# Kernel tuning notes

Measured on AMD Instinct MI355X. Metric: run time of the kernel, lower is better.

Reference implementation:

```python
import jax, jax.numpy as jnp
import numpy as np

B, L, T, V = 64, 512, 1000, 256
E, H, M, S = 256, 512, 80, 128  # text_embed, hidden, n_mels, speaker_dim


def lstm_scan(x, Wih, Whh, b):
    # x: [T, B, D]; torch gate order i, f, g, o; bias = b_ih + b_hh fused
    Bn = x.shape[1]
    Hn = Whh.shape[1]
    h0 = jnp.zeros((Bn, Hn), x.dtype)

    def step(carry, xt):
        h, c = carry
        g = xt @ Wih.T + h @ Whh.T + b
        i, f, gg, o = jnp.split(g, 4, axis=-1)
        c = jax.nn.sigmoid(f) * c + jax.nn.sigmoid(i) * jnp.tanh(gg)
        h = jax.nn.sigmoid(o) * jnp.tanh(c)
        return (h, c), h

    _, ys = jax.lax.scan(step, (h0, h0), x)
    return ys  # [T, B, H]


def setup_inputs() -> dict:
    key = jax.random.key(0)
    ks = jax.random.split(key, 32)
    r = lambda i, shp: (jax.random.normal(ks[i], shp, jnp.float32) * 0.1)
    Hd = H // 2  # 256, per-direction biLSTM hidden
    inp = {
        "text_input": jax.random.randint(ks[0], (B, L), 0, V),
        "speaker_embedding": jax.random.normal(ks[1], (B, S), jnp.float32),
        "target_mel": jax.random.normal(ks[2], (B, T, M), jnp.float32),
        "embed": r(3, (V, E)),
        # bidirectional text LSTM (hidden//2 per direction)
        "enc_Wih_f": r(4, (4 * Hd, E)), "enc_Whh_f": r(5, (4 * Hd, Hd)), "enc_b_f": r(6, (4 * Hd,)),
        "enc_Wih_b": r(7, (4 * Hd, E)), "enc_Whh_b": r(8, (4 * Hd, Hd)), "enc_b_b": r(9, (4 * Hd,)),
        # speaker projection MLP
        "sp_W1": r(10, (H, S)), "sp_b1": r(11, (H,)),
        "sp_W2": r(12, (H, H)), "sp_b2": r(13, (H,)),
        # 2-layer decoder LSTM, input = H + M = 592
        "dec_Wih0": r(14, (4 * H, H + M)), "dec_Whh0": r(15, (4 * H, H)), "dec_b0": r(16, (4 * H,)),
        "dec_Wih1": r(17, (4 * H, H)), "dec_Whh1": r(18, (4 * H, H)), "dec_b1": r(19, (4 * H,)),
        # mel projection MLP
        "mel_W1": r(20, (H, H)), "mel_b1": r(21, (H,)),
        "mel_W2": r(22, (M, H)), "mel_b2": r(23, (M,)),
        # stop token projection
        "stop_W": r(24, (1, H)), "stop_b": r(25, (1,)),
    }
    return inp


def reference(text_input, speaker_embedding, target_mel, embed,
              enc_Wih_f, enc_Whh_f, enc_b_f, enc_Wih_b, enc_Whh_b, enc_b_b,
              sp_W1, sp_b1, sp_W2, sp_b2,
              dec_Wih0, dec_Whh0, dec_b0, dec_Wih1, dec_Whh1, dec_b1,
              mel_W1, mel_b1, mel_W2, mel_b2, stop_W, stop_b):
    # --- text encoder: embedding + biLSTM ---
    x = jnp.swapaxes(embed[text_input], 0, 1)  # [L, B, E]
    fwd = lstm_scan(x, enc_Wih_f, enc_Whh_f, enc_b_f)          # [L, B, H/2]
    bwd = lstm_scan(x[::-1], enc_Wih_b, enc_Whh_b, enc_b_b)[::-1]
    text_encoded = jnp.swapaxes(jnp.concatenate([fwd, bwd], -1), 0, 1)  # [B, L, H]

    # --- speaker projection, broadcast over text length ---
    sp = jax.nn.relu(speaker_embedding @ sp_W1.T + sp_b1) @ sp_W2.T + sp_b2  # [B, H]
    encoder_output = text_encoded + sp[:, None, :]  # [B, L, H]

    # --- teacher-forced decoder: query_t = encoder_output[:, t % L] ---
    idx = jnp.arange(T) % L
    query = encoder_output[:, idx]  # [B, T, H]
    dec_mel_in = jnp.concatenate(
        [jnp.zeros((B, 1, M), target_mel.dtype), target_mel[:, :-1]], axis=1)  # [B, T, M]
    rnn_in = jnp.swapaxes(jnp.concatenate([dec_mel_in, query], -1), 0, 1)  # [T, B, H+M]

    h1 = lstm_scan(rnn_in, dec_Wih0, dec_Whh0, dec_b0)  # [T, B, H]
    h2 = lstm_scan(h1, dec_Wih1, dec_Whh1, dec_b1)      # [T, B, H]
    out = jnp.swapaxes(h2, 0, 1)  # [B, T, H]

    mel_outputs = jax.nn.relu(out @ mel_W1.T + mel_b1) @ mel_W2.T + mel_b2  # [B, T, M]
    stop_outputs = out @ stop_W.T + stop_b  # [B, T, 1]
    return mel_outputs, stop_outputs
```

## Files before the change

kernel.cpp:

```cpp
#include <hip/hip_runtime.h>
#include <cstdint>
#include <cstddef>


#define DEVI __device__ __forceinline__

typedef short bf16x8 __attribute__((ext_vector_type(8)));
typedef float f32x4 __attribute__((ext_vector_type(4)));
typedef unsigned short u16x4 __attribute__((ext_vector_type(4)));

constexpr int B_ = 64, L_ = 512, T_ = 1000, E_ = 256, H_ = 512, M_ = 80, S_ = 128, Hd_ = 256;

DEVI unsigned short f2bs(float f) {
  unsigned u = __builtin_bit_cast(unsigned, f);
  unsigned r = u + 0x7fffu + ((u >> 16) & 1u);
  return (unsigned short)(r >> 16);
}
DEVI float b2f(unsigned short s) { return __builtin_bit_cast(float, (unsigned)s << 16); }
DEVI void split2(float v, unsigned short& hi, unsigned short& lo) {
  hi = f2bs(v);
  lo = f2bs(v - b2f(hi));
}
DEVI float sigm(float x) { x = fminf(fmaxf(x, -30.f), 30.f); return 1.f / (1.f + __expf(-x)); }
DEVI float tanh_(float x) { x = fminf(fmaxf(x, -15.f), 15.f); float e = __expf(2.f * x); return (e - 1.f) / (e + 1.f); }

DEVI f32x4 mfma16(bf16x8 a, bf16x8 b, f32x4 c) {
  return __builtin_amdgcn_mfma_f32_16x16x32_bf16(a, b, c, 0, 0, 0);
}

DEVI void ldg16(bf16x8& r, const unsigned short* p) {
  asm volatile("global_load_dwordx4 %0, %1, off" : "=v"(r) : "v"(p));
}
DEVI void ldc16(bf16x8& r, const unsigned short* p) {
  asm volatile("global_load_dwordx4 %0, %1, off sc0 sc1" : "=v"(r) : "v"(p));
}
DEVI void st4c(unsigned short* p, unsigned v) {
  asm volatile("global_store_dword %0, %1, off sc0 sc1" :: "v"(p), "v"(v));
}
DEVI void sti4c(int* p, int v) {
  asm volatile("global_store_dword %0, %1, off sc0 sc1" :: "v"(p), "v"(v));
}
DEVI void st8c(unsigned short* p, u16x4 v) {
  asm volatile("global_store_dwordx2 %0, %1, off sc0 sc1" :: "v"(p), "v"(v));
}
#define WAITV(N) do { asm volatile("s_waitcnt vmcnt(" #N ")" ::: "memory"); \
                      __builtin_amdgcn_sched_barrier(0); } while (0)
#define VM_DRAIN() WAITV(0)

DEVI void hotwait(const int* p, int target) {
  int v;
  for (;;) {
    asm volatile("global_load_dword %0, %1, off sc0 sc1" : "=v"(v) : "v"(p));
    float x = 0.5f;
#pragma unroll
    for (int i = 0; i < 192; ++i)
      asm volatile("v_fmac_f32 %0, %1, %1" : "+v"(x) : "v"(x));
    asm volatile("" :: "v"(x));
    asm volatile("s_waitcnt vmcnt(0)" ::: "memory");
    __builtin_amdgcn_sched_barrier(0);
    if (v >= target) break;
  }
}

struct Bar { int sub[16][16]; int master[16]; int rel[128][16]; };

template <int NWG, int NSUB>
DEVI void grid_barX(Bar* bb, int step) {
  __shared__ int finS;
  const int tid = threadIdx.x;
  __syncthreads();
  if (tid == 0) {
    finS = 0;
    constexpr int per = NWG / NSUB;
    int old = __hip_atomic_fetch_add(&bb->sub[(int)blockIdx.x % NSUB][0], 1,
                                     __ATOMIC_RELAXED, __HIP_MEMORY_SCOPE_AGENT);
    if (old == per * (step + 1) - 1) {
      int om = __hip_atomic_fetch_add(&bb->master[0], 1,
                                      __ATOMIC_RELAXED, __HIP_MEMORY_SCOPE_AGENT);
      if (om == NSUB * (step + 1) - 1) finS = 1;
    }
  }
  __syncthreads();
  if (finS && tid < NWG) sti4c(&bb->rel[tid][0], step + 1);
  hotwait(&bb->rel[(int)blockIdx.x][0], step + 1);
}

template <int N, class FI, class FM>
DEVI void pipe3(FI issue, FM domf) {
  bf16x8 S0[8], S1[8], S2[8];
  issue(0, S0);
  if constexpr (N > 1) issue(1, S1);
  if constexpr (N > 2) issue(2, S2);
#pragma unroll
  for (int j = 0; j < N; ++j) {
    if (j + 2 < N) { WAITV(16); } else if (j + 1 < N) { WAITV(8); } else { WAITV(0); }
    if (j % 3 == 0)      { domf(j, S0); if (j + 3 < N) issue(j + 3, S0); }
    else if (j % 3 == 1) { domf(j, S1); if (j + 3 < N) issue(j + 3, S1); }
    else                 { domf(j, S2); if (j + 3 < N) issue(j + 3, S2); }
  }
}

__global__ void k_prep(const float* __restrict__ embed, const float* __restrict__ tmel,
                       const float* __restrict__ mw1, const float* __restrict__ mw2,
                       unsigned short* emb_h, unsigned short* emb_l,
                       unsigned short* mel_h, unsigned short* mel_l,
                       unsigned short* w1_bf, unsigned short* w2_bf) {
  const long long stride = (long long)gridDim.x * blockDim.x;
  const long long i0 = (long long)blockIdx.x * blockDim.x + threadIdx.x;
  for (long long i = i0; i < 256 * 256; i += stride) {
    unsigned short h, l; split2(embed[i], h, l);
    emb_h[i] = h; emb_l[i] = l;
  }
  for (long long i = i0; i < (long long)T_ * B_ * 96; i += stride) {
    int c = (int)(i % 96);
    long long tb = i / 96;
    int b = (int)(tb % B_);
    int t = (int)(tb / B_);
    float v = 0.f;
    if (t > 0 && c < 80) v = tmel[((long long)b * T_ + (t - 1)) * M_ + c];
    unsigned short h, l; split2(v, h, l);
    mel_h[i] = h; mel_l[i] = l;
  }
  for (long long i = i0; i < 512 * 512; i += stride) w1_bf[i] = f2bs(mw1[i]);
  for (long long i = i0; i < 80 * 512; i += stride) w2_bf[i] = f2bs(mw2[i]);
}

__global__ void __launch_bounds__(512) k_sp(const float* __restrict__ spk,
                                            const float* __restrict__ w1, const float* __restrict__ b1,
                                            const float* __restrict__ w2, const float* __restrict__ b2,
                                            float* sp) {
  __shared__ float t1[512];
  const int b = blockIdx.x, j = threadIdx.x;
  float a = b1[j];
  const float* sr = spk + b * S_;
  for (int k = 0; k < S_; ++k) a += sr[k] * w1[j * S_ + k];
  t1[j] = fmaxf(a, 0.f);
  __syncthreads();
  float a2 = b2[j];
  for (int k = 0; k < H_; ++k) a2 += t1[k] * w2[j * H_ + k];
  sp[b * H_ + j] = a2;
}

constexpr int ENC_LDS = 2 * 16 * 4 * 64 * 16 + 4 * 64 * 16 * 4 + 256;

__global__ void __launch_bounds__(256, 1) k_enc(
    const int* __restrict__ text,
    const float* __restrict__ WihF, const float* __restrict__ WhhF, const float* __restrict__ bF,
    const float* __restrict__ WihB, const float* __restrict__ WhhB, const float* __restrict__ bB,
    const unsigned short* __restrict__ emb_h, const unsigned short* __restrict__ emb_l,
    const float* __restrict__ sp,
    unsigned short* hencfh, unsigned short* hencfl,
    unsigned short* ench, unsigned short* encl, Bar* bar) {
  extern __shared__ char lds[];
  unsigned short* Wh = (unsigned short*)lds;
  unsigned short* Wl = Wh + 16 * 4 * 64 * 8;
  float* G = (float*)(lds + 2 * 16 * 4 * 64 * 16);
  float* bias = G + 4 * 64 * 16;

  const int wg = blockIdx.x;
  const int dir = wg >> 4;
  const int jhb = (wg & 15) * 16;
  const int tid = threadIdx.x;
  const int wv = tid >> 6, ln = tid & 63, lg = ln >> 4, lr = ln & 15;

  const float* Wih = dir ? WihB : WihF;
  const float* Whh = dir ? WhhB : WhhF;
  const float* bb = dir ? bB : bF;

  for (int s = tid; s < 16 * 4 * 64; s += 256) {
    int kb = s >> 8, g = (s >> 6) & 3, l = s & 63;
    int R = g * Hd_ + jhb + (l & 15);
    int k0 = kb * 32 + (l >> 4) * 8;
    const float* src = (k0 < E_) ? (Wih + (size_t)R * E_ + k0) : (Whh + (size_t)R * Hd_ + (k0 - E_));
    bf16x8 vh, vl;
#pragma unroll
    for (int j = 0; j < 8; ++j) {
      unsigned short a, b; split2(src[j], a, b);
      vh[j] = (short)a; vl[j] = (short)b;
    }
    *(bf16x8*)(Wh + (size_t)s * 8) = vh;
    *(bf16x8*)(Wl + (size_t)s * 8) = vl;
  }
  if (tid < 64) bias[tid] = bb[(tid >> 4) * Hd_ + jhb + (tid & 15)];

  const int eb = tid >> 2, ej0 = (tid & 3) * 4;
  float c4[4] = {0.f, 0.f, 0.f, 0.f};
  float spv[4];
#pragma unroll
  for (int q = 0; q < 4; ++q) spv[q] = sp[eb * H_ + dir * Hd_ + jhb + ej0 + q];

  const int jh = jhb + ej0;
  const size_t fro = ((size_t)((jh >> 5) * 4 + (eb >> 4)) * 64 +
                      (((jh >> 3) & 3) * 16 + (eb & 15))) * 8 + (jh & 7);

  __syncthreads();

  for (int t = 0; t < L_; ++t) {
    const int tpos = dir ? (L_ - 1 - t) : t;
    const unsigned short* hsh = hencfh + ((size_t)((t & 1) * 2 + dir)) * 16384;
    const unsigned short* hsl = hencfl + ((size_t)((t & 1) * 2 + dir)) * 16384;
    unsigned short* hdh = hencfh + ((size_t)(((t + 1) & 1) * 2 + dir)) * 16384;
    unsigned short* hdl = hencfl + ((size_t)(((t + 1) & 1) * 2 + dir)) * 16384;

    for (int i = tid; i < 4096; i += 256) G[i] = bias[((i >> 10) << 4) + (i & 15)];

    int tix[4];
#pragma unroll
    for (int m = 0; m < 4; ++m) tix[m] = text[(16 * m + lr) * L_ + tpos];

    f32x4 acc[4][4];
#pragma unroll
    for (int g = 0; g < 4; ++g)
#pragma unroll
      for (int m = 0; m < 4; ++m) acc[g][m] = (f32x4){0.f, 0.f, 0.f, 0.f};

    auto issue = [&](int j, bf16x8 (&S)[8]) {
      const int kb = wv + 4 * j;
      if (kb < 8) {
        const int k0 = kb * 32 + lg * 8;
#pragma unroll
        for (int m = 0; m < 4; ++m) {
          ldg16(S[m],     emb_h + (size_t)tix[m] * E_ + k0);
          ldg16(S[4 + m], emb_l + (size_t)tix[m] * E_ + k0);
        }
      } else {
        const unsigned short* ph = hsh + ((size_t)((kb - 8) * 4) * 64 + ln) * 8;
        const unsigned short* pl = hsl + ((size_t)((kb - 8) * 4) * 64 + ln) * 8;
#pragma unroll
        for (int m = 0; m < 4; ++m) { ldc16(S[m], ph + m * 512); ldc16(S[4 + m], pl + m * 512); }
      }
    };
    auto domf = [&](int j, bf16x8 (&S)[8]) {
      const int kb = wv + 4 * j;
#pragma unroll
      for (int g = 0; g < 4; ++g) {
        bf16x8 bh = *(bf16x8*)(Wh + ((size_t)(kb * 4 + g) * 64 + ln) * 8);
        bf16x8 bl = *(bf16x8*)(Wl + ((size_t)(kb * 4 + g) * 64 + ln) * 8);
#pragma unroll
        for (int m = 0; m < 4; ++m) {
          acc[g][m] = mfma16(S[m],     bh, acc[g][m]);
          acc[g][m] = mfma16(S[4 + m], bh, acc[g][m]);
          acc[g][m] = mfma16(S[m],     bl, acc[g][m]);
        }
      }
    };
    pipe3<4>(issue, domf);

    __syncthreads();
#pragma unroll
    for (int g = 0; g < 4; ++g)
#pragma unroll
      for (int m = 0; m < 4; ++m)
#pragma unroll
        for (int r = 0; r < 4; ++r)
          atomicAdd(&G[(g * 64 + 16 * m + 4 * lg + r) * 16 + lr], acc[g][m][r]);
    __syncthreads();

    {
      u16x4 hvh, hvl, ovh, ovl;
#pragma unroll
      for (int q = 0; q < 4; ++q) {
        int jj = ej0 + q;
        float gi = G[(0 * 64 + eb) * 16 + jj];
        float gf = G[(1 * 64 + eb) * 16 + jj];
        float gg = G[(2 * 64 + eb) * 16 + jj];
        float go = G[(3 * 64 + eb) * 16 + jj];
        float cn = sigm(gf) * c4[q] + sigm(gi) * tanh_(gg);
        c4[q] = cn;
        float h = sigm(go) * tanh_(cn);
        unsigned short a, b; split2(h, a, b);
        hvh[q] = a; hvl[q] = b;
        float o = h + spv[q];
        split2(o, a, b);
        ovh[q] = a; ovl[q] = b;
      }
      st8c(hdh + fro, hvh);
      st8c(hdl + fro, hvl);
      *(u16x4*)(ench + ((size_t)tpos * B_ + eb) * H_ + dir * Hd_ + jhb + ej0) = ovh;
      *(u16x4*)(encl + ((size_t)tpos * B_ + eb) * H_ + dir * Hd_ + jhb + ej0) = ovl;
    }
    VM_DRAIN();
    grid_barX<32, 8>(bar, t);
  }
}

constexpr int DEC_LDS = 2 * 35 * 2 * 64 * 16 + 4 * 64 * 8 * 4 + 128;

__global__ void __launch_bounds__(256, 1) k_dec(
    const float* __restrict__ Wih0, const float* __restrict__ Whh0, const float* __restrict__ b0,
    const float* __restrict__ Wih1, const float* __restrict__ Whh1, const float* __restrict__ b1,
    const unsigned short* __restrict__ ench, const unsigned short* __restrict__ encl,
    const unsigned short* __restrict__ melh, const unsigned short* __restrict__ mell,
    unsigned short* h0fh, unsigned short* h0fl,
    unsigned short* h1fh, unsigned short* h1fl,
    unsigned short* h2_full, Bar* bar) {
  extern __shared__ char lds[];
  const int wg = blockIdx.x;
  const int layer = wg >> 6;
  const int jcb = (wg & 63) * 8;
  const int tid = threadIdx.x, wv = tid >> 6, ln = tid & 63, lg = ln >> 4, lr = ln & 15;
  const int NKB = layer ? 32 : 35;
  unsigned short* Wh = (unsigned short*)lds;
  unsigned short* Wl = Wh + (size_t)NKB * 2 * 64 * 8;
  float* G = (float*)(lds + (size_t)2 * NKB * 2 * 64 * 16);
  float* bias = G + 4 * 64 * 8;

  if (layer == 0) {
    for (int s = tid; s < 35 * 2 * 64; s += 256) {
      int kb = s >> 7, st = (s >> 6) & 1, l = s & 63;
      int n = l & 15;
      int R = (2 * st + (n >> 3)) * H_ + jcb + (n & 7);
      int k0 = kb * 32 + (l >> 4) * 8;
      bf16x8 vh, vl;
      if (k0 < 96) {
#pragma unroll
        for (int j = 0; j < 8; ++j) {
          int c = k0 + j;
          float v = (c < 80) ? Wih0[(size_t)R * 592 + c] : 0.f;
          unsigned short a, b; split2(v, a, b);
          vh[j] = (short)a; vl[j] = (short)b;
        }
      } else if (k0 < 608) {
        const float* src = Wih0 + (size_t)R * 592 + (k0 - 16);
#pragma unroll
        for (int j = 0; j < 8; ++j) {
          unsigned short a, b; split2(src[j], a, b);
          vh[j] = (short)a; vl[j] = (short)b;
        }
      } else {
        const float* src = Whh0 + (size_t)R * H_ + (k0 - 608);
#pragma unroll
        for (int j = 0; j < 8; ++j) {
          unsigned short a, b; split2(src[j], a, b);
          vh[j] = (short)a; vl[j] = (short)b;
        }
      }
      *(bf16x8*)(Wh + (size_t)s * 8) = vh;
      *(bf16x8*)(Wl + (size_t)s * 8) = vl;
    }
    if (tid < 32) bias[tid] = b0[(tid >> 3) * H_ + jcb + (tid & 7)];
  } else {
    for (int s = tid; s < 32 * 2 * 64; s += 256) {
      int kb = s >> 7, st = (s >> 6) & 1, l = s & 63;
      int n = l & 15;
      int R = (2 * st + (n >> 3)) * H_ + jcb + (n & 7);
      int k0 = kb * 32 + (l >> 4) * 8;
      const float* src = (k0 < 512) ? (Wih1 + (size_t)R * H_ + k0) : (Whh1 + (size_t)R * H_ + (k0 - 512));
      bf16x8 vh, vl;
#pragma unroll
      for (int j = 0; j < 8; ++j) {
        unsigned short a, b; split2(src[j], a, b);
        vh[j] = (short)a; vl[j] = (short)b;
      }
      *(bf16x8*)(Wh + (size_t)s * 8) = vh;
      *(bf16x8*)(Wl + (size_t)s * 8) = vl;
    }
    if (tid < 32) bias[tid] = b1[(tid >> 3) * H_ + jcb + (tid & 7)];
  }

  const int ebd = tid & 63, cc0 = (tid >> 6) * 2;
  float c2[2] = {0.f, 0.f};
  const int j0w = jcb + cc0;
  const size_t frw = ((size_t)((j0w >> 5) * 4 + (ebd >> 4)) * 64 +
                      (((j0w >> 3) & 3) * 16 + (ebd & 15))) * 8 + (j0w & 7);
  __syncthreads();

  for (int tau = 0; tau <= T_; ++tau) {
    const bool active = (layer == 0) ? (tau < T_) : (tau >= 1);
    if (active) {
      const int t = (layer == 0) ? tau : tau - 1;
      for (int i = tid; i < 2048; i += 256) G[i] = bias[((i >> 9) << 3) + (i & 7)];

      f32x4 acc[2][4];
#pragma unroll
      for (int st = 0; st < 2; ++st)
#pragma unroll
        for (int m = 0; m < 4; ++m) acc[st][m] = (f32x4){0.f, 0.f, 0.f, 0.f};

      auto MF = [&](int kb, bf16x8 (&S)[8]) {
#pragma unroll
        for (int st = 0; st < 2; ++st) {
          bf16x8 bh = *(bf16x8*)(Wh + ((size_t)(kb * 2 + st) * 64 + ln) * 8);
          bf16x8 bl = *(bf16x8*)(Wl + ((size_t)(kb * 2 + st) * 64 + ln) * 8);
#pragma unroll
          for (int m = 0; m < 4; ++m) {
            acc[st][m] = mfma16(S[m],     bh, acc[st][m]);
            acc[st][m] = mfma16(S[4 + m], bh, acc[st][m]);
            acc[st][m] = mfma16(S[m],     bl, acc[st][m]);
          }
        }
      };

      if (layer == 0) {
        const int tq = t & (L_ - 1);
        const unsigned short* p0h = h0fh + (size_t)((tau + 1) & 1) * 32768;
        const unsigned short* p0l = h0fl + (size_t)((tau + 1) & 1) * 32768;
        auto issue = [&](int j, bf16x8 (&S)[8]) {
          const int kb = wv + 4 * j;
          const int k0 = kb * 32 + lg * 8;
          if (kb < 3) {
#pragma unroll
            for (int m = 0; m < 4; ++m) {
              ldg16(S[m],     melh + ((size_t)t * B_ + 16 * m + lr) * 96 + k0);
              ldg16(S[4 + m], mell + ((size_t)t * B_ + 16 * m + lr) * 96 + k0);
            }
          } else if (kb < 19) {
            const int k = k0 - 96;
#pragma unroll
            for (int m = 0; m < 4; ++m) {
              ldg16(S[m],     ench + ((size_t)tq * B_ + 16 * m + lr) * H_ + k);
              ldg16(S[4 + m], encl + ((size_t)tq * B_ + 16 * m + lr) * H_ + k);
            }
          } else {
            const unsigned short* ph = p0h + ((size_t)((kb - 19) * 4) * 64 + ln) * 8;
            const unsigned short* pl = p0l + ((size_t)((kb - 19) * 4) * 64 + ln) * 8;
#pragma unroll
            for (int m = 0; m < 4; ++m) { ldc16(S[m], ph + m * 512); ldc16(S[4 + m], pl + m * 512); }
          }
        };
        auto domf = [&](int j, bf16x8 (&S)[8]) { MF(wv + 4 * j, S); };
        if (wv < 3) pipe3<9>(issue, domf);
        else        pipe3<8>(issue, domf);
      } else {
        const unsigned short* q0h = h0fh + (size_t)((tau + 1) & 1) * 32768;
        const unsigned short* q0l = h0fl + (size_t)((tau + 1) & 1) * 32768;
        const unsigned short* q1h = h1fh + (size_t)(tau & 1) * 32768;
        const unsigned short* q1l = h1fl + (size_t)(tau & 1) * 32768;
        auto issue = [&](int j, bf16x8 (&S)[8]) {
          const int kb = wv + 4 * j;
          const unsigned short* ph = (kb < 16) ? (q0h + ((size_t)(kb * 4) * 64 + ln) * 8)
                                               : (q1h + ((size_t)((kb - 16) * 4) * 64 + ln) * 8);
          const unsigned short* pl = (kb < 16) ? (q0l + ((size_t)(kb * 4) * 64 + ln) * 8)
                                               : (q1l + ((size_t)((kb - 16) * 4) * 64 + ln) * 8);
#pragma unroll
          for (int m = 0; m < 4; ++m) { ldc16(S[m], ph + m * 512); ldc16(S[4 + m], pl + m * 512); }
        };
        auto domf = [&](int j, bf16x8 (&S)[8]) { MF(wv + 4 * j, S); };
        pipe3<8>(issue, domf);
      }

      __syncthreads();
#pragma unroll
      for (int st = 0; st < 2; ++st)
#pragma unroll
        for (int m = 0; m < 4; ++m)
#pragma unroll
          for (int r = 0; r < 4; ++r) {
            int g = 2 * st + (lr >> 3), col = lr & 7;
            atomicAdd(&G[(g * 64 + 16 * m + 4 * lg + r) * 8 + col], acc[st][m][r]);
          }
      __syncthreads();

      {
        unsigned short* dh = layer ? (h1fh + (size_t)((tau + 1) & 1) * 32768)
                                   : (h0fh + (size_t)(tau & 1) * 32768);
        unsigned short* dl = layer ? (h1fl + (size_t)((tau + 1) & 1) * 32768)
                                   : (h0fl + (size_t)(tau & 1) * 32768);
        unsigned short hh[2], hl[2];
#pragma unroll
        for (int q = 0; q < 2; ++q) {
          int c = cc0 + q;
          float gi = G[(0 * 64 + ebd) * 8 + c];
          float gf = G[(1 * 64 + ebd) * 8 + c];
          float gg = G[(2 * 64 + ebd) * 8 + c];
          float go = G[(3 * 64 + ebd) * 8 + c];
          float cn = sigm(gf) * c2[q] + sigm(gi) * tanh_(gg);
          c2[q] = cn;
          float h = sigm(go) * tanh_(cn);
          split2(h, hh[q], hl[q]);
        }
        unsigned ph = (unsigned)hh[0] | ((unsigned)hh[1] << 16);
        unsigned pl = (unsigned)hl[0] | ((unsigned)hl[1] << 16);
        st4c(dh + frw, ph);
        st4c(dl + frw, pl);
        if (layer) *(unsigned*)(h2_full + ((size_t)t * B_ + ebd) * H_ + jcb + cc0) = ph;
      }
      VM_DRAIN();
    }
    grid_barX<128, 16>(bar, tau);
  }
}

constexpr int MLP_LDS = 64 * 1024;

__global__ void __launch_bounds__(256) k_mlp(
    const unsigned short* __restrict__ h2_full,
    const unsigned short* __restrict__ w1_bf, const unsigned short* __restrict__ w2_bf,
    const float* __restrict__ mb1, const float* __restrict__ mb2,
    const float* __restrict__ stW, const float* __restrict__ stb, float* out) {
  extern __shared__ char lds[];
  const int t = blockIdx.x;
  const int tid = threadIdx.x, wv = tid >> 6, ln = tid & 63, lg = ln >> 4, lr = ln & 15;
  const unsigned short* A = h2_full + (size_t)t * B_ * H_;

  for (int half = 0; half < 2; ++half) {
    const int nb = wv * 8 + half * 4;
    f32x4 acc[4][4];
#pragma unroll
    for (int nn = 0; nn < 4; ++nn) {
      float bv = mb1[(nb + nn) * 16 + lr];
#pragma unroll
      for (int m = 0; m < 4; ++m) acc[m][nn] = (f32x4){bv, bv, bv, bv};
    }
    for (int kb = 0; kb < 16; ++kb) {
      int k0 = kb * 32 + lg * 8;
      bf16x8 afr[4], bfr[4];
#pragma unroll
      for (int m = 0; m < 4; ++m) afr[m] = *(const bf16x8*)(A + (size_t)(16 * m + lr) * H_ + k0);
#pragma unroll
      for (int nn = 0; nn < 4; ++nn) bfr[nn] = *(const bf16x8*)(w1_bf + (size_t)((nb + nn) * 16 + lr) * H_ + k0);
#pragma unroll
      for (int m = 0; m < 4; ++m)
#pragma unroll
        for (int nn = 0; nn < 4; ++nn) acc[m][nn] = mfma16(afr[m], bfr[nn], acc[m][nn]);
    }
#pragma unroll
    for (int m = 0; m < 4; ++m)
#pragma unroll
      for (int nn = 0; nn < 4; ++nn)
#pragma unroll
        for (int r = 0; r < 4; ++r) {
          int row = 16 * m + 4 * lg + r, col = (nb + nn) * 16 + lr;
          *(unsigned short*)(lds + row * 1024 + ((col * 2) ^ ((row & 7) << 4))) =
              f2bs(fmaxf(acc[m][nn][r], 0.f));
        }
  }
  __syncthreads();

  {
    f32x4 acc2[5];
#pragma unroll
    for (int n = 0; n < 5; ++n) {
      float bv = mb2[n * 16 + lr];
      acc2[n] = (f32x4){bv, bv, bv, bv};
    }
    for (int kb = 0; kb < 16; ++kb) {
      int k0 = kb * 32 + lg * 8;
      int row = 16 * wv + lr;
      bf16x8 afr = *(bf16x8*)(lds + row * 1024 + ((k0 * 2) ^ ((row & 7) << 4)));
#pragma unroll
      for (int n = 0; n < 5; ++n) {
        bf16x8 bfr = *(const bf16x8*)(w2_bf + (size_t)(n * 16 + lr) * H_ + k0);
        acc2[n] = mfma16(afr, bfr, acc2[n]);
      }
    }
#pragma unroll
    for (int n = 0; n < 5; ++n)
#pragma unroll
      for (int r = 0; r < 4; ++r) {
        int b = 16 * wv + 4 * lg + r;
        out[((size_t)b * T_ + t) * M_ + n * 16 + lr] = acc2[n][r];
      }
  }

  if (tid < 64) {
    int b = tid;
    float s = stb[0];
    const unsigned short* hp = A + (size_t)b * H_;
    for (int k = 0; k < H_; ++k) s += b2f(hp[k]) * stW[k];
    out[(size_t)B_ * T_ * M_ + (size_t)b * T_ + t] = s;
  }
}

extern "C" void kernel_launch(void* const* d_in, const int* in_sizes, int n_in,
                              void* d_out, int out_size, void* d_ws, size_t ws_size,
                              hipStream_t stream) {
  (void)in_sizes; (void)n_in; (void)out_size; (void)ws_size;
  const int* text = (const int*)d_in[0];
  const float* spk = (const float*)d_in[1];
  const float* tmel = (const float*)d_in[2];
  const float* embed = (const float*)d_in[3];
  const float* eWihF = (const float*)d_in[4];
  const float* eWhhF = (const float*)d_in[5];
  const float* ebF = (const float*)d_in[6];
  const float* eWihB = (const float*)d_in[7];
  const float* eWhhB = (const float*)d_in[8];
  const float* ebB = (const float*)d_in[9];
  const float* spW1 = (const float*)d_in[10];
  const float* spb1 = (const float*)d_in[11];
  const float* spW2 = (const float*)d_in[12];
  const float* spb2 = (const float*)d_in[13];
  const float* dWih0 = (const float*)d_in[14];
  const float* dWhh0 = (const float*)d_in[15];
  const float* db0 = (const float*)d_in[16];
  const float* dWih1 = (const float*)d_in[17];
  const float* dWhh1 = (const float*)d_in[18];
  const float* db1 = (const float*)d_in[19];
  const float* mW1 = (const float*)d_in[20];
  const float* mb1 = (const float*)d_in[21];
  const float* mW2 = (const float*)d_in[22];
  const float* mb2 = (const float*)d_in[23];
  const float* stW = (const float*)d_in[24];
  const float* stb = (const float*)d_in[25];
  float* out = (float*)d_out;

  char* base = (char*)d_ws;
  size_t off = 0;
  auto carve = [&](size_t bytes) -> void* {
    void* p = base + off;
    off += (bytes + 255) & ~(size_t)255;
    return p;
  };
  Bar* barE = (Bar*)carve(sizeof(Bar));
  Bar* barD = (Bar*)carve(sizeof(Bar));
  unsigned short* h0fh = (unsigned short*)carve((size_t)2 * 32768 * 2);
  unsigned short* h0fl = (unsigned short*)carve((size_t)2 * 32768 * 2);
  unsigned short* h1fh = (unsigned short*)carve((size_t)2 * 32768 * 2);
  unsigned short* h1fl = (unsigned short*)carve((size_t)2 * 32768 * 2);
  unsigned short* hencfh = (unsigned short*)carve((size_t)4 * 16384 * 2);
  unsigned short* hencfl = (unsigned short*)carve((size_t)4 * 16384 * 2);
  const size_t state_bytes = off;
  float* sp = (float*)carve((size_t)B_ * H_ * 4);
  unsigned short* emb_h = (unsigned short*)carve((size_t)256 * 256 * 2);
  unsigned short* emb_l = (unsigned short*)carve((size_t)256 * 256 * 2);
  unsigned short* mel_h = (unsigned short*)carve((size_t)T_ * B_ * 96 * 2);
  unsigned short* mel_l = (unsigned short*)carve((size_t)T_ * B_ * 96 * 2);
  unsigned short* w1_bf = (unsigned short*)carve((size_t)512 * 512 * 2);
  unsigned short* w2_bf = (unsigned short*)carve((size_t)80 * 512 * 2);
  unsigned short* ench = (unsigned short*)carve((size_t)L_ * B_ * H_ * 2);
  unsigned short* encl = (unsigned short*)carve((size_t)L_ * B_ * H_ * 2);
  unsigned short* h2_full = (unsigned short*)carve((size_t)T_ * B_ * H_ * 2);

  hipMemsetAsync(d_ws, 0, state_bytes, stream);

  hipFuncSetAttribute((const void*)k_enc, hipFuncAttributeMaxDynamicSharedMemorySize, ENC_LDS);
  hipFuncSetAttribute((const void*)k_dec, hipFuncAttributeMaxDynamicSharedMemorySize, DEC_LDS);
  hipFuncSetAttribute((const void*)k_mlp, hipFuncAttributeMaxDynamicSharedMemorySize, MLP_LDS);

  k_prep<<<2048, 256, 0, stream>>>(embed, tmel, mW1, mW2, emb_h, emb_l, mel_h, mel_l, w1_bf, w2_bf);
  k_sp<<<64, 512, 0, stream>>>(spk, spW1, spb1, spW2, spb2, sp);
  k_enc<<<32, 256, ENC_LDS, stream>>>(text, eWihF, eWhhF, ebF, eWihB, eWhhB, ebB,
                                      emb_h, emb_l, sp, hencfh, hencfl, ench, encl, barE);
  k_dec<<<128, 256, DEC_LDS, stream>>>(dWih0, dWhh0, db0, dWih1, dWhh1, db1,
                                       ench, encl, mel_h, mel_l,
                                       h0fh, h0fl, h1fh, h1fl, h2_full, barD);
  k_mlp<<<1000, 256, MLP_LDS, stream>>>(h2_full, w1_bf, w2_bf, mb1, mb2, stW, stb, out);
}
```

Before: 36.22 ms.

## Replace grid barriers with per-producer tag flags and 4-deep state ring

```diff
diff --git a/kernel.cpp b/kernel.cpp
--- a/kernel.cpp
+++ b/kernel.cpp
@@ -47,56 +47,46 @@
                       __builtin_amdgcn_sched_barrier(0); } while (0)
 #define VM_DRAIN() WAITV(0)
 
-DEVI void hotwait(const int* p, int target) {
-  int v;
+DEVI void burn64() {
+  float x = 0.5f;
+#pragma unroll
+  for (int i = 0; i < 64; ++i)
+    asm volatile("v_fmac_f32 %0, %1, %1" : "+v"(x) : "v"(x));
+  asm volatile("" :: "v"(x));
+}
+
+DEVI void tagwait1(const int* tags, int idx, int thr) {
+  const int* p = tags + idx;
   for (;;) {
+    int v;
     asm volatile("global_load_dword %0, %1, off sc0 sc1" : "=v"(v) : "v"(p));
-    float x = 0.5f;
-#pragma unroll
-    for (int i = 0; i < 192; ++i)
-      asm volatile("v_fmac_f32 %0, %1, %1" : "+v"(x) : "v"(x));
-    asm volatile("" :: "v"(x));
+    burn64();
     asm volatile("s_waitcnt vmcnt(0)" ::: "memory");
     __builtin_amdgcn_sched_barrier(0);
-    if (v >= target) break;
-  }
-}
-
-struct Bar { int sub[16][16]; int master[16]; int rel[128][16]; };
-
-template <int NWG, int NSUB>
-DEVI void grid_barX(Bar* bb, int step) {
-  __shared__ int finS;
-  const int tid = threadIdx.x;
-  __syncthreads();
-  if (tid == 0) {
-    finS = 0;
-    constexpr int per = NWG / NSUB;
-    int old = __hip_atomic_fetch_add(&bb->sub[(int)blockIdx.x % NSUB][0], 1,
-                                     __ATOMIC_RELAXED, __HIP_MEMORY_SCOPE_AGENT);
-    if (old == per * (step + 1) - 1) {
-      int om = __hip_atomic_fetch_add(&bb->master[0], 1,
-                                      __ATOMIC_RELAXED, __HIP_MEMORY_SCOPE_AGENT);
-      if (om == NSUB * (step + 1) - 1) finS = 1;
-    }
-  }
-  __syncthreads();
-  if (finS && tid < NWG) sti4c(&bb->rel[tid][0], step + 1);
-  hotwait(&bb->rel[(int)blockIdx.x][0], step + 1);
-}
-
-template <int N, class FI, class FM>
-DEVI void pipe3(FI issue, FM domf) {
-  bf16x8 S0[8], S1[8], S2[8];
-  issue(0, S0);
-  if constexpr (N > 1) issue(1, S1);
-  if constexpr (N > 2) issue(2, S2);
-#pragma unroll
-  for (int j = 0; j < N; ++j) {
-    if (j + 2 < N) { WAITV(16); } else if (j + 1 < N) { WAITV(8); } else { WAITV(0); }
-    if (j % 3 == 0)      { domf(j, S0); if (j + 3 < N) issue(j + 3, S0); }
-    else if (j % 3 == 1) { domf(j, S1); if (j + 3 < N) issue(j + 3, S1); }
-    else                 { domf(j, S2); if (j + 3 < N) issue(j + 3, S2); }
+    if (__all(v >= thr)) break;
+  }
+}
+DEVI void tagwait2(const int* t0, const int* t1, int idx, int a, int b) {
+  const int* p0 = t0 + idx;
+  const int* p1 = t1 + idx;
+  for (;;) {
+    int v0, v1;
+    asm volatile("global_load_dword %0, %1, off sc0 sc1" : "=v"(v0) : "v"(p0));
+    asm volatile("global_load_dword %0, %1, off sc0 sc1" : "=v"(v1) : "v"(p1));
+    burn64();
+    asm volatile("s_waitcnt vmcnt(0)" ::: "memory");
+    __builtin_amdgcn_sched_barrier(0);
+    if (__all(v0 >= a) && __all(v1 >= b)) break;
+  }
+}
+DEVI void warwait(const int* cnt, int thr) {
+  for (;;) {
+    int v;
+    asm volatile("global_load_dword %0, %1, off sc0 sc1" : "=v"(v) : "v"(cnt));
+    burn64();
+    asm volatile("s_waitcnt vmcnt(0)" ::: "memory");
+    __builtin_amdgcn_sched_barrier(0);
+    if (v >= thr) break;
   }
 }
 
@@ -150,7 +140,8 @@
     const unsigned short* __restrict__ emb_h, const unsigned short* __restrict__ emb_l,
     const float* __restrict__ sp,
     unsigned short* hencfh, unsigned short* hencfl,
-    unsigned short* ench, unsigned short* encl, Bar* bar) {
+    unsigned short* ench, unsigned short* encl,
+    int* tagHE, int* warE) {
   extern __shared__ char lds[];
   unsigned short* Wh = (unsigned short*)lds;
   unsigned short* Wl = Wh + 16 * 4 * 64 * 8;
@@ -159,7 +150,8 @@
 
   const int wg = blockIdx.x;
   const int dir = wg >> 4;
-  const int jhb = (wg & 15) * 16;
+  const int cg = wg & 15;
+  const int jhb = cg * 16;
   const int tid = threadIdx.x;
   const int wv = tid >> 6, ln = tid & 63, lg = ln >> 4, lr = ln & 15;
 
@@ -197,10 +189,10 @@
 
   for (int t = 0; t < L_; ++t) {
     const int tpos = dir ? (L_ - 1 - t) : t;
-    const unsigned short* hsh = hencfh + ((size_t)((t & 1) * 2 + dir)) * 16384;
-    const unsigned short* hsl = hencfl + ((size_t)((t & 1) * 2 + dir)) * 16384;
-    unsigned short* hdh = hencfh + ((size_t)(((t + 1) & 1) * 2 + dir)) * 16384;
-    unsigned short* hdl = hencfl + ((size_t)(((t + 1) & 1) * 2 + dir)) * 16384;
+    const unsigned short* hsh = hencfh + ((size_t)(((t - 1) & 3) * 2 + dir)) * 16384;
+    const unsigned short* hsl = hencfl + ((size_t)(((t - 1) & 3) * 2 + dir)) * 16384;
+    unsigned short* hdh = hencfh + ((size_t)((t & 3) * 2 + dir)) * 16384;
+    unsigned short* hdl = hencfl + ((size_t)((t & 3) * 2 + dir)) * 16384;
 
     for (int i = tid; i < 4096; i += 256) G[i] = bias[((i >> 10) << 4) + (i & 15)];
 
@@ -214,7 +206,7 @@
 #pragma unroll
       for (int m = 0; m < 4; ++m) acc[g][m] = (f32x4){0.f, 0.f, 0.f, 0.f};
 
-    auto issue = [&](int j, bf16x8 (&S)[8]) {
+    auto issueE = [&](int j, bf16x8 (&S)[8]) {
       const int kb = wv + 4 * j;
       if (kb < 8) {
         const int k0 = kb * 32 + lg * 8;
@@ -230,8 +222,7 @@
         for (int m = 0; m < 4; ++m) { ldc16(S[m], ph + m * 512); ldc16(S[4 + m], pl + m * 512); }
       }
     };
-    auto domf = [&](int j, bf16x8 (&S)[8]) {
-      const int kb = wv + 4 * j;
+    auto MFE = [&](int kb, bf16x8 (&S)[8]) {
 #pragma unroll
       for (int g = 0; g < 4; ++g) {
         bf16x8 bh = *(bf16x8*)(Wh + ((size_t)(kb * 4 + g) * 64 + ln) * 8);
@@ -244,7 +235,17 @@
         }
       }
     };
-    pipe3<4>(issue, domf);
+
+    bf16x8 S0[8], S1[8], S2[8];
+    issueE(0, S0);
+    issueE(1, S1);
+    tagwait1(tagHE, dir * 16 + (ln & 15), t);
+    issueE(2, S2);
+    MFE(wv, S0);
+    issueE(3, S0);
+    MFE(wv + 4, S1);
+    WAITV(8);  MFE(wv + 8, S2);
+    WAITV(0);  MFE(wv + 12, S0);
 
     __syncthreads();
 #pragma unroll
@@ -255,6 +256,8 @@
         for (int r = 0; r < 4; ++r)
           atomicAdd(&G[(g * 64 + 16 * m + 4 * lg + r) * 16 + lr], acc[g][m][r]);
     __syncthreads();
+
+    if (t >= 3) warwait(warE + dir * 16, 16 * (t - 2));
 
     {
       u16x4 hvh, hvl, ovh, ovl;
@@ -280,7 +283,11 @@
       *(u16x4*)(encl + ((size_t)tpos * B_ + eb) * H_ + dir * Hd_ + jhb + ej0) = ovl;
     }
     VM_DRAIN();
-    grid_barX<32, 8>(bar, t);
+    __syncthreads();
+    if (tid == 0) {
+      sti4c(&tagHE[dir * 16 + cg], t + 1);
+      __hip_atomic_fetch_add(&warE[dir * 16], 1, __ATOMIC_RELAXED, __HIP_MEMORY_SCOPE_AGENT);
+    }
   }
 }
 
@@ -293,7 +300,7 @@
     const unsigned short* __restrict__ melh, const unsigned short* __restrict__ mell,
     unsigned short* h0fh, unsigned short* h0fl,
     unsigned short* h1fh, unsigned short* h1fl,
-    unsigned short* h2_full, Bar* bar) {
+    unsigned short* h2_full, int* tagH0, int* tagH1, int* warD) {
   extern __shared__ char lds[];
   const int wg = blockIdx.x;
   const int layer = wg >> 6;
@@ -391,11 +398,13 @@
         }
       };
 
+      bf16x8 S0[8], S1[8], S2[8], S3[8];
+
       if (layer == 0) {
         const int tq = t & (L_ - 1);
-        const unsigned short* p0h = h0fh + (size_t)((tau + 1) & 1) * 32768;
-        const unsigned short* p0l = h0fl + (size_t)((tau + 1) & 1) * 32768;
-        auto issue = [&](int j, bf16x8 (&S)[8]) {
+        const unsigned short* p0h = h0fh + (size_t)((tau - 1) & 3) * 32768;
+        const unsigned short* p0l = h0fl + (size_t)((tau - 1) & 3) * 32768;
+        auto issueL0 = [&](int j, bf16x8 (&S)[8]) {
           const int kb = wv + 4 * j;
           const int k0 = kb * 32 + lg * 8;
           if (kb < 3) {
@@ -418,15 +427,38 @@
             for (int m = 0; m < 4; ++m) { ldc16(S[m], ph + m * 512); ldc16(S[4 + m], pl + m * 512); }
           }
         };
-        auto domf = [&](int j, bf16x8 (&S)[8]) { MF(wv + 4 * j, S); };
-        if (wv < 3) pipe3<9>(issue, domf);
-        else        pipe3<8>(issue, domf);
+        issueL0(0, S0); issueL0(1, S1); issueL0(2, S2);
+        tagwait1(tagH0, ln, tau);
+        MF(wv, S0);      issueL0(3, S0);
+        MF(wv + 4, S1);  issueL0(4, S1);
+        MF(wv + 8, S2);  issueL0(5, S2);
+        if (wv < 3) {
+          constexpr int N = 9;
+#pragma unroll
+          for (int j = 3; j < N; ++j) {
+            if (j + 2 < N) { WAITV(16); } else if (j + 1 < N) { WAITV(8); } else { WAITV(0); }
+            const int kb = wv + 4 * j;
+            if (j % 3 == 0)      { MF(kb, S0); if (j + 3 < N) issueL0(j + 3, S0); }
+            else if (j % 3 == 1) { MF(kb, S1); if (j + 3 < N) issueL0(j + 3, S1); }
+            else                 { MF(kb, S2); if (j + 3 < N) issueL0(j + 3, S2); }
+          }
+        } else {
+          constexpr int N = 8;
+#pragma unroll
+          for (int j = 3; j < N; ++j) {
+            if (j + 2 < N) { WAITV(16); } else if (j + 1 < N) { WAITV(8); } else { WAITV(0); }
+            const int kb = wv + 4 * j;
+            if (j % 3 == 0)      { MF(kb, S0); if (j + 3 < N) issueL0(j + 3, S0); }
+            else if (j % 3 == 1) { MF(kb, S1); if (j + 3 < N) issueL0(j + 3, S1); }
+            else                 { MF(kb, S2); if (j + 3 < N) issueL0(j + 3, S2); }
+          }
+        }
       } else {
-        const unsigned short* q0h = h0fh + (size_t)((tau + 1) & 1) * 32768;
-        const unsigned short* q0l = h0fl + (size_t)((tau + 1) & 1) * 32768;
-        const unsigned short* q1h = h1fh + (size_t)(tau & 1) * 32768;
-        const unsigned short* q1l = h1fl + (size_t)(tau & 1) * 32768;
-        auto issue = [&](int j, bf16x8 (&S)[8]) {
+        const unsigned short* q0h = h0fh + (size_t)((tau - 1) & 3) * 32768;
+        const unsigned short* q0l = h0fl + (size_t)((tau - 1) & 3) * 32768;
+        const unsigned short* q1h = h1fh + (size_t)((tau - 2) & 3) * 32768;
+        const unsigned short* q1l = h1fl + (size_t)((tau - 2) & 3) * 32768;
+        auto issueL1 = [&](int j, bf16x8 (&S)[8]) {
           const int kb = wv + 4 * j;
           const unsigned short* ph = (kb < 16) ? (q0h + ((size_t)(kb * 4) * 64 + ln) * 8)
                                                : (q1h + ((size_t)((kb - 16) * 4) * 64 + ln) * 8);
@@ -435,8 +467,18 @@
 #pragma unroll
           for (int m = 0; m < 4; ++m) { ldc16(S[m], ph + m * 512); ldc16(S[4 + m], pl + m * 512); }
         };
-        auto domf = [&](int j, bf16x8 (&S)[8]) { MF(wv + 4 * j, S); };
-        pipe3<8>(issue, domf);
+        tagwait2(tagH0, tagH1, ln, tau, tau - 1);
+        issueL1(0, S0); issueL1(1, S1); issueL1(2, S2); issueL1(3, S3);
+#pragma unroll
+        for (int j = 0; j < 8; ++j) {
+          if (j + 3 < 8) { WAITV(24); } else if (j + 2 < 8) { WAITV(16); }
+          else if (j + 1 < 8) { WAITV(8); } else { WAITV(0); }
+          const int kb = wv + 4 * j;
+          if ((j & 3) == 0)      { MF(kb, S0); if (j + 4 < 8) issueL1(j + 4, S0); }
+          else if ((j & 3) == 1) { MF(kb, S1); if (j + 4 < 8) issueL1(j + 4, S1); }
+          else if ((j & 3) == 2) { MF(kb, S2); if (j + 4 < 8) issueL1(j + 4, S2); }
+          else                   { MF(kb, S3); if (j + 4 < 8) issueL1(j + 4, S3); }
+        }
       }
 
       __syncthreads();
@@ -451,11 +493,13 @@
           }
       __syncthreads();
 
+      if (tau >= 3) warwait(warD, 128 * (tau - 2));
+
       {
-        unsigned short* dh = layer ? (h1fh + (size_t)((tau + 1) & 1) * 32768)
-                                   : (h0fh + (size_t)(tau & 1) * 32768);
-        unsigned short* dl = layer ? (h1fl + (size_t)((tau + 1) & 1) * 32768)
-                                   : (h0fl + (size_t)(tau & 1) * 32768);
+        unsigned short* dh = layer ? (h1fh + (size_t)((tau - 1) & 3) * 32768)
+                                   : (h0fh + (size_t)(tau & 3) * 32768);
+        unsigned short* dl = layer ? (h1fl + (size_t)((tau - 1) & 3) * 32768)
+                                   : (h0fl + (size_t)(tau & 3) * 32768);
         unsigned short hh[2], hl[2];
 #pragma unroll
         for (int q = 0; q < 2; ++q) {
@@ -476,8 +520,16 @@
         if (layer) *(unsigned*)(h2_full + ((size_t)t * B_ + ebd) * H_ + jcb + cc0) = ph;
       }
       VM_DRAIN();
-    }
-    grid_barX<128, 16>(bar, tau);
+      __syncthreads();
+      if (tid == 0) {
+        if (layer == 0) sti4c(&tagH0[wg], tau + 1);
+        else            sti4c(&tagH1[wg - 64], tau);
+        __hip_atomic_fetch_add(warD, 1, __ATOMIC_RELAXED, __HIP_MEMORY_SCOPE_AGENT);
+      }
+    } else {
+      if (tid == 0)
+        __hip_atomic_fetch_add(warD, 1, __ATOMIC_RELAXED, __HIP_MEMORY_SCOPE_AGENT);
+    }
   }
 }
 
@@ -601,14 +653,17 @@
     off += (bytes + 255) & ~(size_t)255;
     return p;
   };
-  Bar* barE = (Bar*)carve(sizeof(Bar));
-  Bar* barD = (Bar*)carve(sizeof(Bar));
-  unsigned short* h0fh = (unsigned short*)carve((size_t)2 * 32768 * 2);
-  unsigned short* h0fl = (unsigned short*)carve((size_t)2 * 32768 * 2);
-  unsigned short* h1fh = (unsigned short*)carve((size_t)2 * 32768 * 2);
-  unsigned short* h1fl = (unsigned short*)carve((size_t)2 * 32768 * 2);
-  unsigned short* hencfh = (unsigned short*)carve((size_t)4 * 16384 * 2);
-  unsigned short* hencfl = (unsigned short*)carve((size_t)4 * 16384 * 2);
+  int* tagH0 = (int*)carve(64 * 4);
+  int* tagH1 = (int*)carve(64 * 4);
+  int* tagHE = (int*)carve(32 * 4);
+  int* warD  = (int*)carve(16 * 4);
+  int* warE  = (int*)carve(32 * 4);
+  unsigned short* h0fh = (unsigned short*)carve((size_t)4 * 32768 * 2);
+  unsigned short* h0fl = (unsigned short*)carve((size_t)4 * 32768 * 2);
+  unsigned short* h1fh = (unsigned short*)carve((size_t)4 * 32768 * 2);
+  unsigned short* h1fl = (unsigned short*)carve((size_t)4 * 32768 * 2);
+  unsigned short* hencfh = (unsigned short*)carve((size_t)8 * 16384 * 2);
+  unsigned short* hencfl = (unsigned short*)carve((size_t)8 * 16384 * 2);
   const size_t state_bytes = off;
   float* sp = (float*)carve((size_t)B_ * H_ * 4);
   unsigned short* emb_h = (unsigned short*)carve((size_t)256 * 256 * 2);
@@ -630,9 +685,11 @@
   k_prep<<<2048, 256, 0, stream>>>(embed, tmel, mW1, mW2, emb_h, emb_l, mel_h, mel_l, w1_bf, w2_bf);
   k_sp<<<64, 512, 0, stream>>>(spk, spW1, spb1, spW2, spb2, sp);
   k_enc<<<32, 256, ENC_LDS, stream>>>(text, eWihF, eWhhF, ebF, eWihB, eWhhB, ebB,
-                                      emb_h, emb_l, sp, hencfh, hencfl, ench, encl, barE);
+                                      emb_h, emb_l, sp, hencfh, hencfl, ench, encl,
+                                      tagHE, warE);
   k_dec<<<128, 256, DEC_LDS, stream>>>(dWih0, dWhh0, db0, dWih1, dWhh1, db1,
                                        ench, encl, mel_h, mel_l,
-                                       h0fh, h0fl, h1fh, h1fl, h2_full, barD);
+                                       h0fh, h0fl, h1fh, h1fl, h2_full,
+                                       tagH0, tagH1, warD);
   k_mlp<<<1000, 256, MLP_LDS, stream>>>(h2_full, w1_bf, w2_bf, mb1, mb2, stW, stb, out);
 }
```

After: 33.75 ms. -6.8%, faster.
